# Performance work log

Measured on AMD Instinct MI355X. Metric: run time of the kernel, lower is better.

Reference implementation:

```python
import jax, jax.numpy as jnp
import numpy as np

N_CELL = 100_000
N_NET = 100_000
N_PIN = 500_000
N_NN = 200_000
N_PAIR = 500_000
RC, RN, RP = 16, 16, 8   # raw cell/net/pin feats
HC, HN, HP = 64, 64, 8   # hidden cell/net/pin feats


def _seg(x, idx, n):
    return jax.ops.segment_sum(x, idx, num_segments=n)


def _ssp(x):  # DGL ShiftedSoftplus used inside CFConv
    return jax.nn.softplus(x) - jnp.log(2.0)


def _graph_conv(x_src, src, dst, n_src, n_dst, W, b):
    # DGL GraphConv, norm='both': c_src = out_deg^-1/2, c_dst = in_deg^-1/2, degrees clamped to >=1
    ones = jnp.ones(src.shape[0], x_src.dtype)
    cs = jnp.clip(_seg(ones, src, n_src), 1.0) ** -0.5
    cd = jnp.clip(_seg(ones, dst, n_dst), 1.0) ** -0.5
    msg = _seg((x_src * cs[:, None])[src], dst, n_dst) * cd[:, None]
    return msg @ W + b


def setup_inputs() -> dict:
    key = jax.random.key(0)
    ks = jax.random.split(key, 40)
    f = lambda i, s: jax.random.normal(ks[i], s, jnp.float32)
    p = lambda i, s: jax.random.normal(ks[i], s, jnp.float32) * 0.05
    ri = lambda i, s, hi: jax.random.randint(ks[i], s, 0, hi)
    return dict(
        cell_feat=f(0, (N_CELL, RC)),
        net_feat=f(1, (N_NET, RN)),
        pin_feat=f(2, (N_PIN, RP)),
        cell_lin_w=p(3, (RC, HC)), cell_lin_b=p(4, (HC,)),
        net_lin_w=p(5, (RN, HN)), net_lin_b=p(6, (HN,)),
        pin_lin_w=p(7, (RP, HP)), pin_lin_b=p(8, (HP,)),
        pins_w=p(9, (HC, HN)), pins_b=p(10, (HN,)),
        father_w=p(11, (HN, HN)), father_b=p(12, (HN,)),
        son_w=p(13, (HN, HN)), son_b=p(14, (HN,)),
        cf_node_w=p(15, (HN, HC)), cf_node_b=p(16, (HC,)),
        cf_e1_w=p(17, (RP, HC)), cf_e1_b=p(18, (HC,)),
        cf_e2_w=p(19, (HC, HC)), cf_e2_b=p(20, (HC,)),
        cf_out_w=p(21, (HC, HC)), cf_out_b=p(22, (HC,)),
        net_dis_w=p(23, (2 * HN, 1)), net_dis_b=p(24, (1,)),
        net_angle_w=p(25, (2 * HN, 1)), net_angle_b=p(26, (1,)),
        pin_dis_w=p(27, (HC + HP + HN, 1)), pin_dis_b=p(28, (1,)),
        pin_angle_w=p(29, (HC + HP + HN, 1)), pin_angle_b=p(30, (1,)),
        pin_net=ri(31, (N_PIN,), N_NET),
        pin_cell=ri(32, (N_PIN,), N_CELL),
        nn_src=ri(33, (N_NN,), N_NET),
        nn_dst=ri(34, (N_NN,), N_NET),
        net_net_pairs=ri(35, (N_PAIR, 2), N_NET),
    )


def reference(cell_feat, net_feat, pin_feat,
              cell_lin_w, cell_lin_b, net_lin_w, net_lin_b, pin_lin_w, pin_lin_b,
              pins_w, pins_b, father_w, father_b, son_w, son_b,
              cf_node_w, cf_node_b, cf_e1_w, cf_e1_b, cf_e2_w, cf_e2_b, cf_out_w, cf_out_b,
              net_dis_w, net_dis_b, net_angle_w, net_angle_b,
              pin_dis_w, pin_dis_b, pin_angle_w, pin_angle_b,
              pin_net, pin_cell, nn_src, nn_dst, net_net_pairs):
    h_cell = jnp.tanh(cell_feat @ cell_lin_w + cell_lin_b)
    h_net = jnp.tanh(net_feat @ net_lin_w + net_lin_b)
    h_pin = jnp.tanh(pin_feat @ pin_lin_w + pin_lin_b)

    # HeteroGraphConv with aggregate='max' (all relations read the PRE-update h)
    net_pins = _graph_conv(h_cell, pin_cell, pin_net, N_CELL, N_NET, pins_w, pins_b)   # cell->net
    net_fa = _graph_conv(h_net, nn_src, nn_dst, N_NET, N_NET, father_w, father_b)      # net->net
    net_so = _graph_conv(h_net, nn_dst, nn_src, N_NET, N_NET, son_w, son_b)            # reversed
    h_net2 = jnp.maximum(jnp.maximum(net_pins, net_fa), net_so)

    # CFConv net->cell; NOTE: original passes RAW pin_feat as edge feats
    e = _ssp(_ssp(pin_feat @ cf_e1_w + cf_e1_b) @ cf_e2_w + cf_e2_b)   # [P, HC]
    hv = h_net @ cf_node_w + cf_node_b                                  # [Nn, HC]
    h_cell2 = _ssp(_seg(hv[pin_net] * e, pin_cell, N_CELL) @ cf_out_w + cf_out_b)

    # gather-based pairwise readouts
    npair = jnp.concatenate([h_net2[net_net_pairs[:, 0]], h_net2[net_net_pairs[:, 1]]], axis=-1)
    npc = jnp.concatenate([h_net2[pin_net], h_pin, h_cell2[pin_cell]], axis=-1)
    net_dis = jax.nn.softplus(npair @ net_dis_w + net_dis_b)[:, 0]
    net_angle = (npair @ net_angle_w + net_angle_b)[:, 0]
    pin_dis = jax.nn.softplus(npc @ pin_dis_w + pin_dis_b)[:, 0]
    pin_angle = (npc @ pin_angle_w + pin_angle_b)[:, 0]
    return (net_dis, net_angle, pin_dis, pin_angle)
```

## Files before the change

### kernel.cpp

```cpp
#include <hip/hip_runtime.h>
#include <math.h>

#define NCELL 100000
#define NNET  100000
#define NPIN  500000
#define NNN   200000
#define NPAIR 500000
#define NSCAN (4 * NNET)
#define SCAN_BLOCKS ((NSCAN + 1023) / 1024)
#define PART_SZ ((NNET + 7) / 8)

typedef __attribute__((ext_vector_type(8))) short short8;
typedef __attribute__((ext_vector_type(4))) float f32x4;
typedef unsigned short u16;
typedef unsigned int u32;
typedef unsigned long long u64;

__device__ __forceinline__ u16 f2bf(float x) {
    union { float f; u32 u; } v; v.f = x;
    u32 r = (v.u + 0x7FFF + ((v.u >> 16) & 1)) >> 16;
    return (u16)r;
}
__device__ __forceinline__ float bf2f(u16 u) {
    union { u32 u; float f; } v; v.u = ((u32)u) << 16; return v.f;
}
__device__ __forceinline__ u32 cvtpk(float lo, float hi) {
    u32 r;
    asm("v_cvt_pk_bf16_f32 %0, %1, %2" : "=v"(r) : "v"(lo), "v"(hi));
    return r;
}
__device__ __forceinline__ u16 f2bf_fast(float v) {
    return (u16)(cvtpk(v, v) & 0xffffu);
}
__device__ __forceinline__ float plo(u32 h) { return bf2f((u16)(h & 0xffff)); }
__device__ __forceinline__ float phi(u32 h) { return bf2f((u16)(h >> 16)); }

__device__ __forceinline__ float softplusf(float x) {
    return fmaxf(x, 0.f) + __logf(1.f + __expf(-fabsf(x)));
}
__device__ __forceinline__ float sspf(float x) {
    return softplusf(x) - 0.69314718055994530942f;
}
__device__ __forceinline__ float ftanh(float x) {
    float xc = fminf(fmaxf(x, -9.f), 9.f);
    float e = __expf(2.f * xc);
    return (e - 1.f) * __builtin_amdgcn_rcpf(e + 1.f);
}

__device__ __forceinline__ short8 load_bfrag(const float* __restrict__ W,
                                             int kt, int nt, int lane) {
    int k0 = kt * 32 + ((lane >> 4) & 3) * 8;
    int c = nt * 16 + (lane & 15);
    short8 f;
#pragma unroll
    for (int j = 0; j < 8; j++) f[j] = (short)f2bf(W[(k0 + j) * 64 + c]);
    return f;
}

__global__ void k_degrees(const int* __restrict__ pin_cell, const int* __restrict__ pin_net,
                          const int* __restrict__ nn_src, const int* __restrict__ nn_dst,
                          u32* __restrict__ cnt,
                          u32* __restrict__ rankNp, u32* __restrict__ rankC,
                          u32* __restrict__ rankD, u32* __restrict__ rankS) {
    int i = blockIdx.x * blockDim.x + threadIdx.x;
    if (i < NPIN) {
        rankNp[i] = atomicAdd(&cnt[pin_net[i]], 1u);
        rankC[i]  = atomicAdd(&cnt[NNET + pin_cell[i]], 1u);
    }
    if (i < NNN) {
        rankD[i] = atomicAdd(&cnt[2 * NNET + nn_dst[i]], 1u);
        rankS[i] = atomicAdd(&cnt[3 * NNET + nn_src[i]], 1u);
    }
}

__global__ __launch_bounds__(256) void k_lin16_all(
    const float* __restrict__ cf, const float* __restrict__ nf,
    const float* __restrict__ Wc, const float* __restrict__ bc,
    const float* __restrict__ Wn, const float* __restrict__ bn,
    u16* __restrict__ h_cell, u16* __restrict__ h_net) {
    int tid = threadIdx.x, lane = tid & 63, w = tid >> 6;
    float wc[16], wn[16];
#pragma unroll
    for (int k = 0; k < 16; k++) { wc[k] = Wc[k * 64 + lane]; wn[k] = Wn[k * 64 + lane]; }
    float bC = bc[lane], bN = bn[lane];
    int wave = blockIdx.x * 4 + w, nw = gridDim.x * 4;
    for (int r = wave; r < NCELL; r += nw) {
        const float4* ip = (const float4*)(cf + (size_t)r * 16);
        float4 a = ip[0], bv = ip[1], c = ip[2], d = ip[3];
        float acc = bC;
        acc = fmaf(a.x, wc[0], acc);  acc = fmaf(a.y, wc[1], acc);
        acc = fmaf(a.z, wc[2], acc);  acc = fmaf(a.w, wc[3], acc);
        acc = fmaf(bv.x, wc[4], acc); acc = fmaf(bv.y, wc[5], acc);
        acc = fmaf(bv.z, wc[6], acc); acc = fmaf(bv.w, wc[7], acc);
        acc = fmaf(c.x, wc[8], acc);  acc = fmaf(c.y, wc[9], acc);
        acc = fmaf(c.z, wc[10], acc); acc = fmaf(c.w, wc[11], acc);
        acc = fmaf(d.x, wc[12], acc); acc = fmaf(d.y, wc[13], acc);
        acc = fmaf(d.z, wc[14], acc); acc = fmaf(d.w, wc[15], acc);
        float v = ftanh(acc);
        float vp = __shfl_xor(v, 1, 64);
        if (!(lane & 1))
            *(u32*)(h_cell + (size_t)r * 64 + lane) = cvtpk(v, vp);
    }
    for (int r = wave; r < NNET; r += nw) {
        const float4* ip = (const float4*)(nf + (size_t)r * 16);
        float4 a = ip[0], bv = ip[1], c = ip[2], d = ip[3];
        float acc = bN;
        acc = fmaf(a.x, wn[0], acc);  acc = fmaf(a.y, wn[1], acc);
        acc = fmaf(a.z, wn[2], acc);  acc = fmaf(a.w, wn[3], acc);
        acc = fmaf(bv.x, wn[4], acc); acc = fmaf(bv.y, wn[5], acc);
        acc = fmaf(bv.z, wn[6], acc); acc = fmaf(bv.w, wn[7], acc);
        acc = fmaf(c.x, wn[8], acc);  acc = fmaf(c.y, wn[9], acc);
        acc = fmaf(c.z, wn[10], acc); acc = fmaf(c.w, wn[11], acc);
        acc = fmaf(d.x, wn[12], acc); acc = fmaf(d.y, wn[13], acc);
        acc = fmaf(d.z, wn[14], acc); acc = fmaf(d.w, wn[15], acc);
        float v = ftanh(acc);
        float vp = __shfl_xor(v, 1, 64);
        if (!(lane & 1))
            *(u32*)(h_net + (size_t)r * 64 + lane) = cvtpk(v, vp);
    }
}

__global__ __launch_bounds__(256) void k_scan1(const u32* __restrict__ in,
                                               u32* __restrict__ out, u32* __restrict__ bsum,
                                               float* __restrict__ deg) {
    __shared__ u32 sc[256];
    int t = threadIdx.x;
    int base = blockIdx.x * 1024 + t * 4;
    u32 v0 = base + 0 < NSCAN ? in[base + 0] : 0;
    u32 v1 = base + 1 < NSCAN ? in[base + 1] : 0;
    u32 v2 = base + 2 < NSCAN ? in[base + 2] : 0;
    u32 v3 = base + 3 < NSCAN ? in[base + 3] : 0;
    if (base + 0 < NSCAN) deg[base + 0] = rsqrtf((float)max(v0, 1u));
    if (base + 1 < NSCAN) deg[base + 1] = rsqrtf((float)max(v1, 1u));
    if (base + 2 < NSCAN) deg[base + 2] = rsqrtf((float)max(v2, 1u));
    if (base + 3 < NSCAN) deg[base + 3] = rsqrtf((float)max(v3, 1u));
    u32 s = v0 + v1 + v2 + v3;
    sc[t] = s; __syncthreads();
    for (int off = 1; off < 256; off <<= 1) {
        u32 x = (t >= off) ? sc[t - off] : 0; __syncthreads();
        sc[t] += x; __syncthreads();
    }
    u32 excl = sc[t] - s;
    if (base + 0 < NSCAN) out[base + 0] = excl;
    if (base + 1 < NSCAN) out[base + 1] = excl + v0;
    if (base + 2 < NSCAN) out[base + 2] = excl + v0 + v1;
    if (base + 3 < NSCAN) out[base + 3] = excl + v0 + v1 + v2;
    if (t == 255) bsum[blockIdx.x] = sc[255];
}

__global__ __launch_bounds__(512) void k_scan2(u32* __restrict__ bsum) {
    __shared__ u32 sc[512];
    int t = threadIdx.x;
    u32 v = (t < SCAN_BLOCKS) ? bsum[t] : 0;
    sc[t] = v; __syncthreads();
    for (int off = 1; off < 512; off <<= 1) {
        u32 x = (t >= off) ? sc[t - off] : 0; __syncthreads();
        sc[t] += x; __syncthreads();
    }
    if (t < SCAN_BLOCKS) bsum[t] = sc[t] - v;
}

__global__ __launch_bounds__(256) void k_scan3(u32* __restrict__ S, const u32* __restrict__ bsum) {
    int i = blockIdx.x * blockDim.x + threadIdx.x;
    if (i < NSCAN) S[i] = S[i] + bsum[i >> 10];
    if (i == 0) S[NSCAN] = 2u * NPIN + 2u * NNN;
}

__global__ __launch_bounds__(256) void k_place_part(
    const int* __restrict__ pin_cell, const int* __restrict__ pin_net,
    const int* __restrict__ nn_src, const int* __restrict__ nn_dst,
    const u32* __restrict__ S,
    const u32* __restrict__ rankNp, const u32* __restrict__ rankC,
    const u32* __restrict__ rankD, const u32* __restrict__ rankS,
    u32* __restrict__ colC, u64* __restrict__ colPN,
    u32* __restrict__ colS, u32* __restrict__ colD) {
    int part = blockIdx.x & 7;
    int grp = blockIdx.x >> 3;
    int ngrp = gridDim.x >> 3;
    int lo = part * PART_SZ, hi = lo + PART_SZ;
    int stride = ngrp * 256;
    for (int e = grp * 256 + threadIdx.x; e < NPIN; e += stride) {
        int n = pin_net[e], c = pin_cell[e];
        if (n >= lo && n < hi)
            colC[S[n] + rankNp[e]] = (u32)c;
        if (c >= lo && c < hi)
            colPN[S[NNET + c] + rankC[e] - NPIN] = (u64)(u32)e | ((u64)(u32)n << 32);
    }
    for (int i = grp * 256 + threadIdx.x; i < NNN; i += stride) {
        int s = nn_src[i], d = nn_dst[i];
        if (d >= lo && d < hi)
            colS[S[2 * NNET + d] + rankD[i] - 2u * NPIN] = (u32)s;
        if (s >= lo && s < hi)
            colD[S[3 * NNET + s] + rankS[i] - (2u * NPIN + NNN)] = (u32)d;
    }
}

__global__ __launch_bounds__(256, 4) void k_emlp(
    const float* __restrict__ pin_feat, const u64* __restrict__ colPN,
    const float* __restrict__ E1, const float* __restrict__ b1,
    const float* __restrict__ E2, const float* __restrict__ b2,
    u16* __restrict__ etab) {
    __shared__ __align__(16) u16 sm[4][1024];
    int tid = threadIdx.x, lane = tid & 63, w = tid >> 6;
    int l15 = lane & 15, g = (lane >> 4) & 3;
    short8 B1[4];
#pragma unroll
    for (int nt = 0; nt < 4; nt++) {
        short8 f = {0, 0, 0, 0, 0, 0, 0, 0};
        if (lane < 16) {
            int c = nt * 16 + l15;
#pragma unroll
            for (int j = 0; j < 8; j++) f[j] = (short)f2bf(E1[j * 64 + c]);
        }
        B1[nt] = f;
    }
    short8 B2[2][4];
#pragma unroll
    for (int kt = 0; kt < 2; kt++)
#pragma unroll
        for (int nt = 0; nt < 4; nt++) B2[kt][nt] = load_bfrag(E2, kt, nt, lane);
    float bb1[4], bb2[4];
#pragma unroll
    for (int nt = 0; nt < 4; nt++) {
        bb1[nt] = b1[nt * 16 + l15];
        bb2[nt] = b2[nt * 16 + l15];
    }
    int wave = blockIdx.x * 4 + w, nwave = gridDim.x * 4;
    const int ntile = NPIN >> 4;
    f32x4 z = {0.f, 0.f, 0.f, 0.f};
    for (int t = wave; t < ntile; t += nwave) {
        int P = t << 4;
        short8 a1 = {0, 0, 0, 0, 0, 0, 0, 0};
        if (lane < 16) {
            u32 p = (u32)colPN[P + lane];
            const float4* q = (const float4*)(pin_feat + (size_t)p * 8);
            float4 u0 = q[0], u1 = q[1];
            u32 w01 = cvtpk(u0.x, u0.y), w23 = cvtpk(u0.z, u0.w);
            u32 w45 = cvtpk(u1.x, u1.y), w67 = cvtpk(u1.z, u1.w);
            a1[0] = (short)(w01 & 0xffff); a1[1] = (short)(w01 >> 16);
            a1[2] = (short)(w23 & 0xffff); a1[3] = (short)(w23 >> 16);
            a1[4] = (short)(w45 & 0xffff); a1[5] = (short)(w45 >> 16);
            a1[6] = (short)(w67 & 0xffff); a1[7] = (short)(w67 >> 16);
        }
#pragma unroll
        for (int nt = 0; nt < 4; nt++) {
            f32x4 c1 = __builtin_amdgcn_mfma_f32_16x16x32_bf16(a1, B1[nt], z, 0, 0, 0);
#pragma unroll
            for (int r = 0; r < 4; r++) {
                int row = g * 4 + r;
                int col = nt * 16 + l15;
                sm[w][row * 64 + (col ^ ((row & 7) << 3))] = f2bf_fast(sspf(c1[r] + bb1[nt]));
            }
        }
        short8 a2[2];
#pragma unroll
        for (int kt = 0; kt < 2; kt++) {
            int idx = l15 * 64 + ((kt * 32 + g * 8) ^ ((l15 & 7) << 3));
            a2[kt] = *(const short8*)&sm[w][idx];
        }
#pragma unroll
        for (int nt = 0; nt < 4; nt++) {
            f32x4 e = __builtin_amdgcn_mfma_f32_16x16x32_bf16(a2[0], B2[0][nt], z, 0, 0, 0);
            e = __builtin_amdgcn_mfma_f32_16x16x32_bf16(a2[1], B2[1][nt], e, 0, 0, 0);
#pragma unroll
            for (int r = 0; r < 4; r++) {
                float v = sspf(e[r] + bb2[nt]);
                float vp = __shfl_xor(v, 1, 64);
                if (!(lane & 1))
                    *(u32*)(etab + (size_t)(P + g * 4 + r) * 64 + nt * 16 + l15) = cvtpk(v, vp);
            }
        }
    }
}

__global__ __launch_bounds__(256, 4) void k_mm64hv(
    const u16* __restrict__ in, const float* __restrict__ W,
    const float* __restrict__ b, u16* __restrict__ out, int n) {
    int tid = threadIdx.x, lane = tid & 63, w = tid >> 6;
    int l15 = lane & 15, g = (lane >> 4) & 3;
    short8 Bf[2][4];
    float bias[4];
#pragma unroll
    for (int kt = 0; kt < 2; kt++)
#pragma unroll
        for (int nt = 0; nt < 4; nt++) Bf[kt][nt] = load_bfrag(W, kt, nt, lane);
#pragma unroll
    for (int nt = 0; nt < 4; nt++) bias[nt] = b[nt * 16 + l15];
    int wave = blockIdx.x * 4 + w, nwave = gridDim.x * 4;
    int ntile = n >> 4;
    f32x4 z = {0.f, 0.f, 0.f, 0.f};
    for (int t = wave; t < ntile; t += nwave) {
        int R = t << 4;
        const u16* rb = in + (size_t)(R + l15) * 64;
        short8 a0 = *(const short8*)(rb + g * 8);
        short8 a1 = *(const short8*)(rb + 32 + g * 8);
#pragma unroll
        for (int nt = 0; nt < 4; nt++) {
            f32x4 acc = __builtin_amdgcn_mfma_f32_16x16x32_bf16(a0, Bf[0][nt], z, 0, 0, 0);
            acc = __builtin_amdgcn_mfma_f32_16x16x32_bf16(a1, Bf[1][nt], acc, 0, 0, 0);
#pragma unroll
            for (int r = 0; r < 4; r++) {
                float v = acc[r] + bias[nt];
                float vp = __shfl_xor(v, 1, 64);
                if (!(lane & 1))
                    *(u32*)(out + (size_t)(R + g * 4 + r) * 64 + nt * 16 + l15) = cvtpk(v, vp);
            }
        }
    }
}

__global__ __launch_bounds__(256) void k_gatherP(
    const u32* __restrict__ S, const u32* __restrict__ colC,
    const u16* __restrict__ h_cell, const float* __restrict__ rCv,
    u16* __restrict__ accP) {
    int l32 = threadIdx.x & 31, off2 = l32 * 2;
    int slot = blockIdx.x * 8 + (threadIdx.x >> 5), ns = gridDim.x * 8;
    for (int n = slot; n < NNET; n += ns) {
        u32 b0 = S[n], b1 = S[n + 1];
        float fa = 0.f, fb = 0.f, ga = 0.f, gb = 0.f;
        u32 k = b0;
        for (; k + 1 < b1; k += 2) {
            u32 c0 = colC[k], c1 = colC[k + 1];
            float r0 = rCv[c0], r1 = rCv[c1];
            u32 h0 = *(const u32*)(h_cell + (size_t)c0 * 64 + off2);
            u32 h1 = *(const u32*)(h_cell + (size_t)c1 * 64 + off2);
            fa = fmaf(plo(h0), r0, fa); fb = fmaf(phi(h0), r0, fb);
            ga = fmaf(plo(h1), r1, ga); gb = fmaf(phi(h1), r1, gb);
        }
        if (k < b1) {
            u32 c0 = colC[k];
            float r0 = rCv[c0];
            u32 h0 = *(const u32*)(h_cell + (size_t)c0 * 64 + off2);
            fa = fmaf(plo(h0), r0, fa); fb = fmaf(phi(h0), r0, fb);
        }
        *(u32*)(accP + (size_t)n * 64 + off2) = cvtpk(fa + ga, fb + gb);
    }
}

__global__ __launch_bounds__(256) void k_gatherFS(
    const u32* __restrict__ S, const u32* __restrict__ colS, const u32* __restrict__ colD,
    const u16* __restrict__ h_net, const float* __restrict__ rDv, const float* __restrict__ rSv,
    u16* __restrict__ accF, u16* __restrict__ accS) {
    int l32 = threadIdx.x & 31, off2 = l32 * 2;
    int slot = blockIdx.x * 8 + (threadIdx.x >> 5), ns = gridDim.x * 8;
    for (int r = slot; r < 2 * NNET; r += ns) {
        if (r < NNET) {
            int d = r;
            u32 b0 = S[2 * NNET + d] - 2u * NPIN, b1 = S[2 * NNET + d + 1] - 2u * NPIN;
            float fa = 0.f, fb = 0.f, ga = 0.f, gb = 0.f;
            u32 k = b0;
            for (; k + 1 < b1; k += 2) {
                u32 s0 = colS[k], s1 = colS[k + 1];
                float c0 = rSv[s0], c1 = rSv[s1];
                u32 h0 = *(const u32*)(h_net + (size_t)s0 * 64 + off2);
                u32 h1 = *(const u32*)(h_net + (size_t)s1 * 64 + off2);
                fa = fmaf(plo(h0), c0, fa); fb = fmaf(phi(h0), c0, fb);
                ga = fmaf(plo(h1), c1, ga); gb = fmaf(phi(h1), c1, gb);
            }
            if (k < b1) {
                u32 s0 = colS[k];
                float c0 = rSv[s0];
                u32 h0 = *(const u32*)(h_net + (size_t)s0 * 64 + off2);
                fa = fmaf(plo(h0), c0, fa); fb = fmaf(phi(h0), c0, fb);
            }
            *(u32*)(accF + (size_t)d * 64 + off2) = cvtpk(fa + ga, fb + gb);
        } else {
            int s = r - NNET;
            u32 b0 = S[3 * NNET + s] - (2u * NPIN + NNN), b1 = S[3 * NNET + s + 1] - (2u * NPIN + NNN);
            float fa = 0.f, fb = 0.f, ga = 0.f, gb = 0.f;
            u32 k = b0;
            for (; k + 1 < b1; k += 2) {
                u32 d0 = colD[k], d1 = colD[k + 1];
                float c0 = rDv[d0], c1 = rDv[d1];
                u32 h0 = *(const u32*)(h_net + (size_t)d0 * 64 + off2);
                u32 h1 = *(const u32*)(h_net + (size_t)d1 * 64 + off2);
                fa = fmaf(plo(h0), c0, fa); fb = fmaf(phi(h0), c0, fb);
                ga = fmaf(plo(h1), c1, ga); gb = fmaf(phi(h1), c1, gb);
            }
            if (k < b1) {
                u32 d0 = colD[k];
                float c0 = rDv[d0];
                u32 h0 = *(const u32*)(h_net + (size_t)d0 * 64 + off2);
                fa = fmaf(plo(h0), c0, fa); fb = fmaf(phi(h0), c0, fb);
            }
            *(u32*)(accS + (size_t)s * 64 + off2) = cvtpk(fa + ga, fb + gb);
        }
    }
}

__global__ __launch_bounds__(256) void k_gatherCell(
    const u32* __restrict__ S, const u64* __restrict__ colPN,
    const u16* __restrict__ etab, const u16* __restrict__ hv, u16* __restrict__ acc) {
    int l32 = threadIdx.x & 31, off2 = l32 * 2;
    int slot = blockIdx.x * 8 + (threadIdx.x >> 5), ns = gridDim.x * 8;
    for (int c = slot; c < NCELL; c += ns) {
        u32 b0 = S[NNET + c] - NPIN, b1 = S[NNET + c + 1] - NPIN;
        float fa = 0.f, fb = 0.f, ga = 0.f, gb = 0.f;
        u32 k = b0;
        for (; k + 1 < b1; k += 2) {
            u32 n0 = (u32)(colPN[k] >> 32), n1 = (u32)(colPN[k + 1] >> 32);
            u32 e0 = *(const u32*)(etab + (size_t)k * 64 + off2);
            u32 e1 = *(const u32*)(etab + (size_t)(k + 1) * 64 + off2);
            u32 h0 = *(const u32*)(hv + (size_t)n0 * 64 + off2);
            u32 h1 = *(const u32*)(hv + (size_t)n1 * 64 + off2);
            fa = fmaf(plo(e0), plo(h0), fa); fb = fmaf(phi(e0), phi(h0), fb);
            ga = fmaf(plo(e1), plo(h1), ga); gb = fmaf(phi(e1), phi(h1), gb);
        }
        if (k < b1) {
            u32 n0 = (u32)(colPN[k] >> 32);
            u32 e0 = *(const u32*)(etab + (size_t)k * 64 + off2);
            u32 h0 = *(const u32*)(hv + (size_t)n0 * 64 + off2);
            fa = fmaf(plo(e0), plo(h0), fa); fb = fmaf(phi(e0), phi(h0), fb);
        }
        *(u32*)(acc + (size_t)c * 64 + off2) = cvtpk(fa + ga, fb + gb);
    }
}

__global__ __launch_bounds__(256, 2) void k_combine3(
    const u16* __restrict__ A0, const float* __restrict__ W0, const float* __restrict__ b0,
    const u16* __restrict__ A1, const float* __restrict__ W1, const float* __restrict__ b1,
    const u16* __restrict__ A2, const float* __restrict__ W2, const float* __restrict__ b2,
    const float* __restrict__ sc0, const float* __restrict__ sc1, const float* __restrict__ sc2,
    const float* __restrict__ ndw, const float* __restrict__ naw,
    const float* __restrict__ pdw, const float* __restrict__ paw,
    float* __restrict__ ntab, int n) {
    int tid = threadIdx.x, lane = tid & 63, w = tid >> 6;
    int l15 = lane & 15, g = (lane >> 4) & 3;
    const float* Ws[3] = {W0, W1, W2};
    const float* bs[3] = {b0, b1, b2};
    const u16* As[3] = {A0, A1, A2};
    short8 Bf[3][2][4];
    float bias[3][4];
#pragma unroll
    for (int rel = 0; rel < 3; rel++) {
#pragma unroll
        for (int kt = 0; kt < 2; kt++)
#pragma unroll
            for (int nt = 0; nt < 4; nt++) Bf[rel][kt][nt] = load_bfrag(Ws[rel], kt, nt, lane);
#pragma unroll
        for (int nt = 0; nt < 4; nt++) bias[rel][nt] = bs[rel][nt * 16 + l15];
    }
    float wt[6][4];
#pragma unroll
    for (int nt = 0; nt < 4; nt++) {
        int c = nt * 16 + l15;
        wt[0][nt] = ndw[c];      wt[1][nt] = naw[c];
        wt[2][nt] = ndw[64 + c]; wt[3][nt] = naw[64 + c];
        wt[4][nt] = pdw[c];      wt[5][nt] = paw[c];
    }
    int wave = blockIdx.x * 4 + w, nwave = gridDim.x * 4;
    int ntile = n >> 4;
    f32x4 z = {0.f, 0.f, 0.f, 0.f};
    for (int t = wave; t < ntile; t += nwave) {
        int R = t << 4;
        int rowA = R + l15;
        float s0a[4], s1a[4], s2a[4];
        *(float4*)s0a = *(const float4*)(sc0 + R + g * 4);
        *(float4*)s1a = *(const float4*)(sc1 + R + g * 4);
        *(float4*)s2a = *(const float4*)(sc2 + R + g * 4);
        f32x4 res[4];
#pragma unroll
        for (int rel = 0; rel < 3; rel++) {
            const u16* rb = As[rel] + (size_t)rowA * 64;
            short8 a0 = *(const short8*)(rb + g * 8);
            short8 a1 = *(const short8*)(rb + 32 + g * 8);
            const float* sa = (rel == 0) ? s0a : (rel == 1) ? s1a : s2a;
#pragma unroll
            for (int nt = 0; nt < 4; nt++) {
                f32x4 acc = __builtin_amdgcn_mfma_f32_16x16x32_bf16(a0, Bf[rel][0][nt], z, 0, 0, 0);
                acc = __builtin_amdgcn_mfma_f32_16x16x32_bf16(a1, Bf[rel][1][nt], acc, 0, 0, 0);
                if (rel == 0) {
#pragma unroll
                    for (int r = 0; r < 4; r++) res[nt][r] = sa[r] * acc[r] + bias[0][nt];
                } else {
#pragma unroll
                    for (int r = 0; r < 4; r++)
                        res[nt][r] = fmaxf(res[nt][r], sa[r] * acc[r] + bias[rel][nt]);
                }
            }
        }
#pragma unroll
        for (int r = 0; r < 4; r++) {
            float a0 = 0.f, a1 = 0.f, a2 = 0.f, a3 = 0.f, a4 = 0.f, a5 = 0.f;
#pragma unroll
            for (int nt = 0; nt < 4; nt++) {
                float v = res[nt][r];
                a0 = fmaf(v, wt[0][nt], a0);
                a1 = fmaf(v, wt[1][nt], a1);
                a2 = fmaf(v, wt[2][nt], a2);
                a3 = fmaf(v, wt[3][nt], a3);
                a4 = fmaf(v, wt[4][nt], a4);
                a5 = fmaf(v, wt[5][nt], a5);
            }
#pragma unroll
            for (int off = 1; off < 16; off <<= 1) {
                a0 += __shfl_xor(a0, off, 64);
                a1 += __shfl_xor(a1, off, 64);
                a2 += __shfl_xor(a2, off, 64);
                a3 += __shfl_xor(a3, off, 64);
                a4 += __shfl_xor(a4, off, 64);
                a5 += __shfl_xor(a5, off, 64);
            }
            if (l15 == 0) {
                float* tp = ntab + (size_t)(R + g * 4 + r) * 8;
                *(float2*)tp = float2{a0, a1};
                *(float2*)(tp + 2) = float2{a2, a3};
                *(float2*)(tp + 4) = float2{a4, a5};
            }
        }
    }
}

__global__ __launch_bounds__(256, 3) void k_mm64c(
    const u16* __restrict__ in, const float* __restrict__ W, const float* __restrict__ b,
    const float* __restrict__ pdw, const float* __restrict__ paw,
    float* __restrict__ ctab, int n) {
    int tid = threadIdx.x, lane = tid & 63, w = tid >> 6;
    int l15 = lane & 15, g = (lane >> 4) & 3;
    short8 Bf[2][4];
    float bias[4], wdv[4], wav[4];
#pragma unroll
    for (int kt = 0; kt < 2; kt++)
#pragma unroll
        for (int nt = 0; nt < 4; nt++) Bf[kt][nt] = load_bfrag(W, kt, nt, lane);
#pragma unroll
    for (int nt = 0; nt < 4; nt++) {
        int c = nt * 16 + l15;
        bias[nt] = b[c];
        wdv[nt] = pdw[72 + c];
        wav[nt] = paw[72 + c];
    }
    int wave = blockIdx.x * 4 + w, nwave = gridDim.x * 4;
    int ntile = n >> 4;
    f32x4 z = {0.f, 0.f, 0.f, 0.f};
    for (int t = wave; t < ntile; t += nwave) {
        int R = t << 4;
        const u16* rb = in + (size_t)(R + l15) * 64;
        short8 a0 = *(const short8*)(rb + g * 8);
        short8 a1 = *(const short8*)(rb + 32 + g * 8);
        float sd[4] = {0.f, 0.f, 0.f, 0.f}, sa[4] = {0.f, 0.f, 0.f, 0.f};
#pragma unroll
        for (int nt = 0; nt < 4; nt++) {
            f32x4 acc = __builtin_amdgcn_mfma_f32_16x16x32_bf16(a0, Bf[0][nt], z, 0, 0, 0);
            acc = __builtin_amdgcn_mfma_f32_16x16x32_bf16(a1, Bf[1][nt], acc, 0, 0, 0);
#pragma unroll
            for (int r = 0; r < 4; r++) {
                float v = sspf(acc[r] + bias[nt]);
                sd[r] = fmaf(v, wdv[nt], sd[r]);
                sa[r] = fmaf(v, wav[nt], sa[r]);
            }
        }
#pragma unroll
        for (int r = 0; r < 4; r++) {
            float d = sd[r], a = sa[r];
#pragma unroll
            for (int off = 1; off < 16; off <<= 1) {
                d += __shfl_xor(d, off, 64);
                a += __shfl_xor(a, off, 64);
            }
            if (l15 == 0)
                *(float2*)(ctab + (size_t)(R + g * 4 + r) * 2) = float2{d, a};
        }
    }
}

__global__ __launch_bounds__(256) void k_readout(
    const int* __restrict__ pairs,
    const float* __restrict__ pin_feat,
    const int* __restrict__ pin_net, const int* __restrict__ pin_cell,
    const float* __restrict__ ntab, const float* __restrict__ ctab,
    const float* __restrict__ plw, const float* __restrict__ plb,
    const float* __restrict__ pdw, const float* __restrict__ paw,
    const float* __restrict__ nbd, const float* __restrict__ nba,
    const float* __restrict__ pbd, const float* __restrict__ pba,
    float* __restrict__ out) {
    int i = blockIdx.x * blockDim.x + threadIdx.x;
    if (i < NPAIR) {
        int p0 = pairs[2 * i], p1 = pairs[2 * i + 1];
        float2 x0 = *(const float2*)(ntab + (size_t)p0 * 8);
        float2 x1 = *(const float2*)(ntab + (size_t)p1 * 8 + 2);
        out[i] = softplusf(x0.x + x1.x + nbd[0]);
        out[NPAIR + i] = x0.y + x1.y + nba[0];
    } else if (i < NPAIR + NPIN) {
        int p = i - NPAIR;
        int n = pin_net[p], c = pin_cell[p];
        float2 ns = *(const float2*)(ntab + (size_t)n * 8 + 4);
        float2 cs = *(const float2*)(ctab + (size_t)c * 2);
        float pf[8];
        *(float4*)pf = *(const float4*)(pin_feat + (size_t)p * 8);
        *(float4*)(pf + 4) = *(const float4*)(pin_feat + (size_t)p * 8 + 4);
        float sd = ns.x + cs.x + pbd[0];
        float sa = ns.y + cs.y + pba[0];
#pragma unroll
        for (int j = 0; j < 8; j++) {
            float a = plb[j];
#pragma unroll
            for (int k = 0; k < 8; k++) a = fmaf(pf[k], plw[k * 8 + j], a);
            float hp = ftanh(a);
            sd = fmaf(hp, pdw[64 + j], sd);
            sa = fmaf(hp, paw[64 + j], sa);
        }
        out[2 * NPAIR + p] = softplusf(sd);
        out[2 * NPAIR + NPIN + p] = sa;
    }
}

extern "C" void kernel_launch(void* const* d_in, const int* in_sizes, int n_in,
                              void* d_out, int out_size, void* d_ws, size_t ws_size,
                              hipStream_t stream) {
    const float* cell_feat = (const float*)d_in[0];
    const float* net_feat  = (const float*)d_in[1];
    const float* pin_feat  = (const float*)d_in[2];
    const float* cell_lin_w = (const float*)d_in[3];
    const float* cell_lin_b = (const float*)d_in[4];
    const float* net_lin_w  = (const float*)d_in[5];
    const float* net_lin_b  = (const float*)d_in[6];
    const float* pin_lin_w  = (const float*)d_in[7];
    const float* pin_lin_b  = (const float*)d_in[8];
    const float* pins_w   = (const float*)d_in[9];
    const float* pins_b   = (const float*)d_in[10];
    const float* father_w = (const float*)d_in[11];
    const float* father_b = (const float*)d_in[12];
    const float* son_w    = (const float*)d_in[13];
    const float* son_b    = (const float*)d_in[14];
    const float* cf_node_w = (const float*)d_in[15];
    const float* cf_node_b = (const float*)d_in[16];
    const float* cf_e1_w  = (const float*)d_in[17];
    const float* cf_e1_b  = (const float*)d_in[18];
    const float* cf_e2_w  = (const float*)d_in[19];
    const float* cf_e2_b  = (const float*)d_in[20];
    const float* cf_out_w = (const float*)d_in[21];
    const float* cf_out_b = (const float*)d_in[22];
    const float* net_dis_w   = (const float*)d_in[23];
    const float* net_dis_b   = (const float*)d_in[24];
    const float* net_angle_w = (const float*)d_in[25];
    const float* net_angle_b = (const float*)d_in[26];
    const float* pin_dis_w   = (const float*)d_in[27];
    const float* pin_dis_b   = (const float*)d_in[28];
    const float* pin_angle_w = (const float*)d_in[29];
    const float* pin_angle_b = (const float*)d_in[30];
    const int* pin_net = (const int*)d_in[31];
    const int* pin_cell = (const int*)d_in[32];
    const int* nn_src = (const int*)d_in[33];
    const int* nn_dst = (const int*)d_in[34];
    const int* pairs = (const int*)d_in[35];

    u16* ws16 = (u16*)d_ws;
    const size_t SZ = (size_t)NNET * 64;
    u16* h_cell   = ws16;
    u16* acc_cell = ws16;
    u16* h_net    = ws16 + SZ;
    u16* accP     = ws16 + 2 * SZ;
    u16* accF     = ws16 + 3 * SZ;
    u16* accS     = ws16 + 4 * SZ;
    u16* etab     = ws16 + 5 * SZ;
    u16* hv       = ws16 + 10 * SZ;
    u32* tail = (u32*)(ws16 + 11 * SZ);
    u32* cnt    = tail;
    u32* Sarr   = cnt + NSCAN;
    u32* rankNp = Sarr + NSCAN + 2;
    u32* rankC  = rankNp + NPIN;
    u32* rankD  = rankC + NPIN;
    u32* rankS  = rankD + NNN;
    u32* colC   = rankS + NNN;
    u32* colS   = colC + NPIN;
    u32* colD   = colS + NNN;
    u64* colPN  = (u64*)(colD + NNN);
    u32* bsum   = (u32*)(colPN + NPIN);
    float* deg  = (float*)(bsum + 512);
    float* rNp = deg;
    float* rC  = deg + NNET;
    float* rD  = deg + 2 * NNET;
    float* rS  = deg + 3 * NNET;
    float* ntab = deg + NSCAN;
    float* ctab = ntab + (size_t)NNET * 8;

    hipMemsetAsync(cnt, 0, NSCAN * sizeof(u32), stream);

    k_degrees<<<(NPIN + 255) / 256, 256, 0, stream>>>(
        pin_cell, pin_net, nn_src, nn_dst, cnt, rankNp, rankC, rankD, rankS);
    k_lin16_all<<<2048, 256, 0, stream>>>(cell_feat, net_feat,
                                          cell_lin_w, cell_lin_b, net_lin_w, net_lin_b,
                                          h_cell, h_net);

    k_scan1<<<SCAN_BLOCKS, 256, 0, stream>>>(cnt, Sarr, bsum, deg);
    k_scan2<<<1, 512, 0, stream>>>(bsum);
    k_scan3<<<(NSCAN + 255) / 256, 256, 0, stream>>>(Sarr, bsum);
    k_place_part<<<2048, 256, 0, stream>>>(pin_cell, pin_net, nn_src, nn_dst,
                                           Sarr, rankNp, rankC, rankD, rankS,
                                           colC, colPN, colS, colD);

    k_emlp<<<2048, 256, 0, stream>>>(pin_feat, colPN, cf_e1_w, cf_e1_b, cf_e2_w, cf_e2_b, etab);
    k_mm64hv<<<1024, 256, 0, stream>>>(h_net, cf_node_w, cf_node_b, hv, NNET);
    k_gatherP<<<2048, 256, 0, stream>>>(Sarr, colC, h_cell, rC, accP);
    k_gatherFS<<<2048, 256, 0, stream>>>(Sarr, colS, colD, h_net, rD, rS, accF, accS);

    k_combine3<<<512, 256, 0, stream>>>(accP, pins_w, pins_b,
                                        accF, father_w, father_b,
                                        accS, son_w, son_b,
                                        rNp, rD, rS,
                                        net_dis_w, net_angle_w, pin_dis_w, pin_angle_w,
                                        ntab, NNET);

    k_gatherCell<<<2048, 256, 0, stream>>>(Sarr, colPN, etab, hv, acc_cell);

    k_mm64c<<<512, 256, 0, stream>>>(acc_cell, cf_out_w, cf_out_b,
                                     pin_dis_w, pin_angle_w, ctab, NCELL);

    float* out = (float*)d_out;
    k_readout<<<(NPAIR + NPIN + 255) / 256, 256, 0, stream>>>(
        pairs, pin_feat, pin_net, pin_cell, ntab, ctab,
        pin_lin_w, pin_lin_b, pin_dis_w, pin_angle_w,
        net_dis_b, net_angle_b, pin_dis_b, pin_angle_b, out);
}
```

Measured before the change: 308.4 us.

## Fuse edge MLP with cell gather using in-tile segmented reduction and bf16 atomics

The edge-MLP kernel now multiplies each edge result by the gathered net features `hv[pin_net]` in place. It reduces the 16 rows of each tile by cell index in LDS. Cells that lie wholly inside a tile are stored directly; boundary segments are added with packed bf16 global atomics. This removes the per-pin edge table write and re-read and the separate gather-cell kernel. The cost is an extra memset of the cell accumulator, atomic traffic and reduced precision from bf16 atomic accumulation, and it relies on wave-synchronous LDS access without barriers.

```diff
diff --git a/kernel.cpp b/kernel.cpp
--- a/kernel.cpp
+++ b/kernel.cpp
@@ -34,6 +34,10 @@
 }
 __device__ __forceinline__ float plo(u32 h) { return bf2f((u16)(h & 0xffff)); }
 __device__ __forceinline__ float phi(u32 h) { return bf2f((u16)(h >> 16)); }
+__device__ __forceinline__ void pk_add(u16* addr, u32 data) {
+    asm volatile("global_atomic_pk_add_bf16 %0, %1, off"
+                 :: "v"((unsigned long long)(uintptr_t)addr), "v"(data));
+}
 
 __device__ __forceinline__ float softplusf(float x) {
     return fmaxf(x, 0.f) + __logf(1.f + __expf(-fabsf(x)));
@@ -172,7 +176,7 @@
     const u32* __restrict__ S,
     const u32* __restrict__ rankNp, const u32* __restrict__ rankC,
     const u32* __restrict__ rankD, const u32* __restrict__ rankS,
-    u32* __restrict__ colC, u64* __restrict__ colPN,
+    u32* __restrict__ colC, u64* __restrict__ colPNC,
     u32* __restrict__ colS, u32* __restrict__ colD) {
     int part = blockIdx.x & 7;
     int grp = blockIdx.x >> 3;
@@ -184,7 +188,8 @@
         if (n >= lo && n < hi)
             colC[S[n] + rankNp[e]] = (u32)c;
         if (c >= lo && c < hi)
-            colPN[S[NNET + c] + rankC[e] - NPIN] = (u64)(u32)e | ((u64)(u32)n << 32);
+            colPNC[S[NNET + c] + rankC[e] - NPIN] =
+                (u64)(u32)e | ((u64)(u32)n << 20) | ((u64)(u32)c << 40);
     }
     for (int i = grp * 256 + threadIdx.x; i < NNN; i += stride) {
         int s = nn_src[i], d = nn_dst[i];
@@ -195,12 +200,14 @@
     }
 }
 
-__global__ __launch_bounds__(256, 4) void k_emlp(
-    const float* __restrict__ pin_feat, const u64* __restrict__ colPN,
+__global__ __launch_bounds__(256, 4) void k_emlp_fused(
+    const float* __restrict__ pin_feat, const u64* __restrict__ colPNC,
     const float* __restrict__ E1, const float* __restrict__ b1,
     const float* __restrict__ E2, const float* __restrict__ b2,
-    u16* __restrict__ etab) {
+    const u16* __restrict__ hv, u16* __restrict__ acc) {
     __shared__ __align__(16) u16 sm[4][1024];
+    __shared__ float smf[4][16][64];
+    __shared__ u64 smc[4][16];
     int tid = threadIdx.x, lane = tid & 63, w = tid >> 6;
     int l15 = lane & 15, g = (lane >> 4) & 3;
     short8 B1[4];
@@ -232,7 +239,9 @@
         int P = t << 4;
         short8 a1 = {0, 0, 0, 0, 0, 0, 0, 0};
         if (lane < 16) {
-            u32 p = (u32)colPN[P + lane];
+            u64 v = colPNC[P + lane];
+            smc[w][lane] = v;
+            u32 p = (u32)(v & 0xFFFFFu);
             const float4* q = (const float4*)(pin_feat + (size_t)p * 8);
             float4 u0 = q[0], u1 = q[1];
             u32 w01 = cvtpk(u0.x, u0.y), w23 = cvtpk(u0.z, u0.w);
@@ -258,17 +267,47 @@
             int idx = l15 * 64 + ((kt * 32 + g * 8) ^ ((l15 & 7) << 3));
             a2[kt] = *(const short8*)&sm[w][idx];
         }
+        f32x4 ef[4];
 #pragma unroll
         for (int nt = 0; nt < 4; nt++) {
             f32x4 e = __builtin_amdgcn_mfma_f32_16x16x32_bf16(a2[0], B2[0][nt], z, 0, 0, 0);
             e = __builtin_amdgcn_mfma_f32_16x16x32_bf16(a2[1], B2[1][nt], e, 0, 0, 0);
 #pragma unroll
-            for (int r = 0; r < 4; r++) {
-                float v = sspf(e[r] + bb2[nt]);
-                float vp = __shfl_xor(v, 1, 64);
-                if (!(lane & 1))
-                    *(u32*)(etab + (size_t)(P + g * 4 + r) * 64 + nt * 16 + l15) = cvtpk(v, vp);
-            }
+            for (int r = 0; r < 4; r++) ef[nt][r] = sspf(e[r] + bb2[nt]);
+        }
+#pragma unroll
+        for (int r = 0; r < 4; r++) {
+            u64 v = smc[w][g * 4 + r];
+            u32 net = (u32)((v >> 20) & 0xFFFFFu);
+#pragma unroll
+            for (int nt = 0; nt < 4; nt++) {
+                float h = bf2f(hv[(size_t)net * 64 + nt * 16 + l15]);
+                smf[w][g * 4 + r][nt * 16 + l15] = ef[nt][r] * h;
+            }
+        }
+        float a = smf[w][0][lane];
+        u32 prev = (u32)(smc[w][0] >> 40);
+        int r0 = 0;
+#pragma unroll
+        for (int r = 1; r < 16; r++) {
+            u32 cr = (u32)(smc[w][r] >> 40);
+            if (cr != prev) {
+                if (r0 > 0) {
+                    acc[(size_t)prev * 64 + lane] = f2bf_fast(a);
+                } else {
+                    float ap = __shfl_xor(a, 1, 64);
+                    if (!(lane & 1)) pk_add(acc + (size_t)prev * 64 + lane, cvtpk(a, ap));
+                }
+                a = smf[w][r][lane];
+                prev = cr;
+                r0 = r;
+            } else {
+                a += smf[w][r][lane];
+            }
+        }
+        {
+            float ap = __shfl_xor(a, 1, 64);
+            if (!(lane & 1)) pk_add(acc + (size_t)prev * 64 + lane, cvtpk(a, ap));
         }
     }
 }
@@ -385,34 +424,6 @@
             }
             *(u32*)(accS + (size_t)s * 64 + off2) = cvtpk(fa + ga, fb + gb);
         }
-    }
-}
-
-__global__ __launch_bounds__(256) void k_gatherCell(
-    const u32* __restrict__ S, const u64* __restrict__ colPN,
-    const u16* __restrict__ etab, const u16* __restrict__ hv, u16* __restrict__ acc) {
-    int l32 = threadIdx.x & 31, off2 = l32 * 2;
-    int slot = blockIdx.x * 8 + (threadIdx.x >> 5), ns = gridDim.x * 8;
-    for (int c = slot; c < NCELL; c += ns) {
-        u32 b0 = S[NNET + c] - NPIN, b1 = S[NNET + c + 1] - NPIN;
-        float fa = 0.f, fb = 0.f, ga = 0.f, gb = 0.f;
-        u32 k = b0;
-        for (; k + 1 < b1; k += 2) {
-            u32 n0 = (u32)(colPN[k] >> 32), n1 = (u32)(colPN[k + 1] >> 32);
-            u32 e0 = *(const u32*)(etab + (size_t)k * 64 + off2);
-            u32 e1 = *(const u32*)(etab + (size_t)(k + 1) * 64 + off2);
-            u32 h0 = *(const u32*)(hv + (size_t)n0 * 64 + off2);
-            u32 h1 = *(const u32*)(hv + (size_t)n1 * 64 + off2);
-            fa = fmaf(plo(e0), plo(h0), fa); fb = fmaf(phi(e0), phi(h0), fb);
-            ga = fmaf(plo(e1), plo(h1), ga); gb = fmaf(phi(e1), phi(h1), gb);
-        }
-        if (k < b1) {
-            u32 n0 = (u32)(colPN[k] >> 32);
-            u32 e0 = *(const u32*)(etab + (size_t)k * 64 + off2);
-            u32 h0 = *(const u32*)(hv + (size_t)n0 * 64 + off2);
-            fa = fmaf(plo(e0), plo(h0), fa); fb = fmaf(phi(e0), phi(h0), fb);
-        }
-        *(u32*)(acc + (size_t)c * 64 + off2) = cvtpk(fa + ga, fb + gb);
     }
 }
 
@@ -648,14 +659,13 @@
     u16* ws16 = (u16*)d_ws;
     const size_t SZ = (size_t)NNET * 64;
     u16* h_cell   = ws16;
-    u16* acc_cell = ws16;
     u16* h_net    = ws16 + SZ;
     u16* accP     = ws16 + 2 * SZ;
     u16* accF     = ws16 + 3 * SZ;
     u16* accS     = ws16 + 4 * SZ;
-    u16* etab     = ws16 + 5 * SZ;
-    u16* hv       = ws16 + 10 * SZ;
-    u32* tail = (u32*)(ws16 + 11 * SZ);
+    u16* acc_cell = ws16 + 5 * SZ;
+    u16* hv       = ws16 + 6 * SZ;
+    u32* tail = (u32*)(ws16 + 7 * SZ);
     u32* cnt    = tail;
     u32* Sarr   = cnt + NSCAN;
     u32* rankNp = Sarr + NSCAN + 2;
@@ -665,8 +675,8 @@
     u32* colC   = rankS + NNN;
     u32* colS   = colC + NPIN;
     u32* colD   = colS + NNN;
-    u64* colPN  = (u64*)(colD + NNN);
-    u32* bsum   = (u32*)(colPN + NPIN);
+    u64* colPNC = (u64*)(colD + NNN);
+    u32* bsum   = (u32*)(colPNC + NPIN);
     float* deg  = (float*)(bsum + 512);
     float* rNp = deg;
     float* rC  = deg + NNET;
@@ -676,6 +686,7 @@
     float* ctab = ntab + (size_t)NNET * 8;
 
     hipMemsetAsync(cnt, 0, NSCAN * sizeof(u32), stream);
+    hipMemsetAsync(acc_cell, 0, SZ * sizeof(u16), stream);
 
     k_degrees<<<(NPIN + 255) / 256, 256, 0, stream>>>(
         pin_cell, pin_net, nn_src, nn_dst, cnt, rankNp, rankC, rankD, rankS);
@@ -688,12 +699,15 @@
     k_scan3<<<(NSCAN + 255) / 256, 256, 0, stream>>>(Sarr, bsum);
     k_place_part<<<2048, 256, 0, stream>>>(pin_cell, pin_net, nn_src, nn_dst,
                                            Sarr, rankNp, rankC, rankD, rankS,
-                                           colC, colPN, colS, colD);
-
-    k_emlp<<<2048, 256, 0, stream>>>(pin_feat, colPN, cf_e1_w, cf_e1_b, cf_e2_w, cf_e2_b, etab);
+                                           colC, colPNC, colS, colD);
+
     k_mm64hv<<<1024, 256, 0, stream>>>(h_net, cf_node_w, cf_node_b, hv, NNET);
     k_gatherP<<<2048, 256, 0, stream>>>(Sarr, colC, h_cell, rC, accP);
     k_gatherFS<<<2048, 256, 0, stream>>>(Sarr, colS, colD, h_net, rD, rS, accF, accS);
+
+    k_emlp_fused<<<2048, 256, 0, stream>>>(pin_feat, colPNC,
+                                           cf_e1_w, cf_e1_b, cf_e2_w, cf_e2_b,
+                                           hv, acc_cell);
 
     k_combine3<<<512, 256, 0, stream>>>(accP, pins_w, pins_b,
                                         accF, father_w, father_b,
@@ -702,8 +716,6 @@
                                         net_dis_w, net_angle_w, pin_dis_w, pin_angle_w,
                                         ntab, NNET);
 
-    k_gatherCell<<<2048, 256, 0, stream>>>(Sarr, colPN, etab, hv, acc_cell);
-
     k_mm64c<<<512, 256, 0, stream>>>(acc_cell, cf_out_w, cf_out_b,
                                      pin_dis_w, pin_angle_w, ctab, NCELL);
 
```

Result: faster. 288.5 us (-6.5%).
